# Optimization experiments

Hardware: AMD Instinct MI355X
Metric: run time of the kernel (lower is better)

## Reference

```python
import jax, jax.numpy as jnp
import numpy as np

NUM_HEADS = 32
NUM_KV_HEADS = 8
HEAD_DIM = 128
ROPE_BASE = 10000.0


def _rope_tables(seq_len, head_dim, dtype):
    inv_freq = 1.0 / (ROPE_BASE ** (jnp.arange(0, head_dim, 2, dtype=jnp.float32) / head_dim))
    t = jnp.arange(seq_len, dtype=jnp.float32)
    freqs = jnp.einsum('i,j->ij', t, inv_freq)          # [S, D/2]
    emb = jnp.concatenate([freqs, freqs], axis=-1)      # [S, D]
    return jnp.cos(emb).astype(dtype), jnp.sin(emb).astype(dtype)


def _rotate_half(x):
    x1, x2 = jnp.split(x, 2, axis=-1)
    return jnp.concatenate([-x2, x1], axis=-1)


def _apply_rope(x, cos, sin):
    # x: [B, H, S, D]; cos/sin: [S, D] broadcast over batch and heads
    return x * cos[None, None, :, :] + _rotate_half(x) * sin[None, None, :, :]


def setup_inputs() -> dict:
    key = jax.random.key(0)
    k1, k2, k3, k4, k5 = jax.random.split(key, 5)
    B, S, H = 1, 2048, 4096
    scale = 0.02
    return {
        'hidden_states': jax.random.normal(k1, (B, S, H), dtype=jnp.float32),
        'Wq': jax.random.normal(k2, (4096, 4096), dtype=jnp.float32) * scale,
        'Wk': jax.random.normal(k3, (1024, 4096), dtype=jnp.float32) * scale,
        'Wv': jax.random.normal(k4, (1024, 4096), dtype=jnp.float32) * scale,
        'Wo': jax.random.normal(k5, (4096, 4096), dtype=jnp.float32) * scale,
    }


def reference(hidden_states, Wq, Wk, Wv, Wo):
    B, S, hidden = hidden_states.shape
    n_rep = NUM_HEADS // NUM_KV_HEADS

    # projections (torch Linear: y = x @ W.T)
    q = (hidden_states @ Wq.T).reshape(B, S, NUM_HEADS, HEAD_DIM).transpose(0, 2, 1, 3)
    k = (hidden_states @ Wk.T).reshape(B, S, NUM_KV_HEADS, HEAD_DIM).transpose(0, 2, 1, 3)
    v = (hidden_states @ Wv.T).reshape(B, S, NUM_KV_HEADS, HEAD_DIM).transpose(0, 2, 1, 3)

    # RoPE: init path with no past -> query/key position ids both arange(S)
    cos, sin = _rope_tables(S, HEAD_DIM, hidden_states.dtype)
    q = _apply_rope(q, cos, sin)
    k = _apply_rope(k, cos, sin)

    # repeat_kv: [B, Hkv, S, D] -> [B, H, S, D]
    k = jnp.repeat(k, n_rep, axis=1)
    v = jnp.repeat(v, n_rep, axis=1)

    # manual attention with causal mask
    scores = jnp.einsum('bhqd,bhkd->bhqk', q, k) / jnp.sqrt(jnp.float32(HEAD_DIM)).astype(q.dtype)
    causal = jnp.tril(jnp.ones((S, S), dtype=bool))
    scores = jnp.where(causal[None, None, :, :], scores, jnp.finfo(scores.dtype).min)
    probs = jax.nn.softmax(scores, axis=-1)

    out = jnp.einsum('bhqk,bhkd->bhqd', probs, v)        # [B, H, S, D]
    out = out.transpose(0, 2, 1, 3).reshape(B, S, hidden)
    return out @ Wo.T
```

## Files before the change

### kernel.cpp

```cpp
#include <hip/hip_runtime.h>
#include <hip/hip_bf16.h>

typedef __attribute__((ext_vector_type(4))) float f32x4;
typedef __attribute__((ext_vector_type(8))) short short8;
typedef __attribute__((ext_vector_type(4))) unsigned int u32x4;

__device__ __forceinline__ unsigned short f2bf(float f) {
  union { float f; unsigned int u; } v; v.f = f;
  unsigned int r = (v.u + 0x7fffu + ((v.u >> 16) & 1u)) >> 16;
  return (unsigned short)r;
}
__device__ __forceinline__ unsigned short f2bf_fast(float f) {
  __hip_bfloat16 h = __float2bfloat16(f);
  return __builtin_bit_cast(unsigned short, h);
}
__device__ __forceinline__ float bf2f(unsigned short h) {
  union { unsigned int u; float f; } v; v.u = ((unsigned int)h) << 16;
  return v.f;
}
__device__ __forceinline__ unsigned int cvt_pk_bf16(float lo, float hi) {
  unsigned int r;
  asm("v_cvt_pk_bf16_f32 %0, %1, %2" : "=v"(r) : "v"(lo), "v"(hi));
  return r;
}

__device__ __forceinline__ void gload_lds16(const void* g, void* l) {
  __builtin_amdgcn_global_load_lds((const __attribute__((address_space(1))) void*)g,
                                   (__attribute__((address_space(3))) void*)l,
                                   16, 0, 0);
}

template <int N>
__device__ __forceinline__ void vmwait() {
  asm volatile("s_waitcnt vmcnt(%0)" :: "n"(N) : "memory");
}

__global__ __launch_bounds__(256) void cvt_all(
    const float* __restrict__ hid, const float* __restrict__ wq,
    const float* __restrict__ wk, const float* __restrict__ wv,
    const float* __restrict__ wo, unsigned short* __restrict__ out) {
  const size_t E0 = 8388608, E1 = 25165824, E2 = 29360128, E3 = 33554432, E4 = 50331648;
  size_t stride = (size_t)gridDim.x * blockDim.x;
  for (size_t i = (size_t)blockIdx.x * blockDim.x + threadIdx.x; i * 4 < E4; i += stride) {
    size_t i4 = i * 4;
    const float* src; size_t rel;
    if (i4 < E0)      { src = hid; rel = i4; }
    else if (i4 < E1) { src = wq;  rel = i4 - E0; }
    else if (i4 < E2) { src = wk;  rel = i4 - E1; }
    else if (i4 < E3) { src = wv;  rel = i4 - E2; }
    else              { src = wo;  rel = i4 - E3; }
    float4 v = *(const float4*)(src + rel);
    ushort4 o;
    o.x = f2bf(v.x); o.y = f2bf(v.y); o.z = f2bf(v.z); o.w = f2bf(v.w);
    *(ushort4*)(out + i4) = o;
  }
}

template <int BM, int BN, bool BF16_OUT>
__global__ __launch_bounds__(256, 2) void gemm_p2(
    const unsigned short* __restrict__ A,
    const unsigned short* __restrict__ B,
    void* __restrict__ Cout, int M, int N, int K) {
  constexpr int BK = 64;
  constexpr int MFRAG = BM / 32;
  constexpr int NFRAG = BN / 32;
  constexpr int ASH = BM * BK;
  constexpr int BSH = BN * BK;
  constexpr int BUF = ASH + BSH;
  constexpr int ALOADS = BM / 32;
  constexpr int BLOADS = BN / 32;
  __shared__ unsigned short lds[2 * BUF];

  const int tid = threadIdx.x;
  const int wave = tid >> 6, lane = tid & 63;
  const int l15 = lane & 15, l4 = lane >> 4;
  const int row0 = blockIdx.y * BM, col0 = blockIdx.x * BN;
  const int mrow0 = (wave >> 1) * (BM / 2);
  const int ncol0 = (wave & 1) * (BN / 2);
  const int NT = K >> 6;
  const int srow = tid >> 3;
  const int scol = ((tid & 7) ^ (srow & 7)) * 8;

  f32x4 zv = {0.f, 0.f, 0.f, 0.f};
  f32x4 acc[MFRAG][NFRAG];
#pragma unroll
  for (int m = 0; m < MFRAG; ++m)
#pragma unroll
    for (int n = 0; n < NFRAG; ++n) acc[m][n] = zv;

  auto stage = [&](int t) {
    unsigned short* buf = &lds[(t & 1) * BUF];
    const int k0 = t * BK;
#pragma unroll
    for (int i = 0; i < ALOADS; ++i)
      gload_lds16(A + (size_t)(row0 + i * 32 + srow) * K + k0 + scol,
                  buf + i * 2048 + tid * 8);
#pragma unroll
    for (int i = 0; i < BLOADS; ++i)
      gload_lds16(B + (size_t)(col0 + i * 32 + srow) * K + k0 + scol,
                  buf + ASH + i * 2048 + tid * 8);
  };

  stage(0);

  for (int t = 0; t < NT; ++t) {
    vmwait<0>();
    __builtin_amdgcn_sched_barrier(0);
    __builtin_amdgcn_s_barrier();
    __builtin_amdgcn_sched_barrier(0);
    if (t + 1 < NT) stage(t + 1);

    const unsigned short* Ab = &lds[(t & 1) * BUF];
    const unsigned short* Bb = Ab + ASH;
#pragma unroll
    for (int h = 0; h < 2; ++h) {
      short8 afr[MFRAG], bfr[NFRAG];
#pragma unroll
      for (int m = 0; m < MFRAG; ++m) {
        int row = mrow0 + m * 16 + l15;
        afr[m] = *(const short8*)&Ab[row * 64 + (((h * 4 + l4) ^ (l15 & 7)) * 8)];
      }
#pragma unroll
      for (int n = 0; n < NFRAG; ++n) {
        int row = ncol0 + n * 16 + l15;
        bfr[n] = *(const short8*)&Bb[row * 64 + (((h * 4 + l4) ^ (l15 & 7)) * 8)];
      }
      __builtin_amdgcn_s_setprio(1);
#pragma unroll
      for (int m = 0; m < MFRAG; ++m)
#pragma unroll
        for (int n = 0; n < NFRAG; ++n)
          acc[m][n] = __builtin_amdgcn_mfma_f32_16x16x32_bf16(afr[m], bfr[n], acc[m][n], 0, 0, 0);
      __builtin_amdgcn_s_setprio(0);
    }
    __builtin_amdgcn_sched_barrier(0);
  }

#pragma unroll
  for (int m = 0; m < MFRAG; ++m)
#pragma unroll
    for (int n = 0; n < NFRAG; ++n)
#pragma unroll
      for (int j = 0; j < 4; ++j) {
        int r = row0 + mrow0 + m * 16 + l4 * 4 + j;
        int cc = col0 + ncol0 + n * 16 + l15;
        if constexpr (BF16_OUT)
          ((unsigned short*)Cout)[(size_t)r * N + cc] = f2bf(acc[m][n][j]);
        else
          ((float*)Cout)[(size_t)r * N + cc] = acc[m][n][j];
      }
}

__global__ __launch_bounds__(256) void rope_k(unsigned short* __restrict__ QKV) {
  int idx = blockIdx.x * blockDim.x + threadIdx.x;
  if (idx >= 2048 * 40 * 64) return;
  int j = idx & 63;
  int rest = idx >> 6;
  int slot = rest % 40;
  int s = rest / 40;
  int doff = (slot < 32) ? slot * 128 : 4096 + (slot - 32) * 128;
  unsigned short* p = QKV + (size_t)s * 6144 + doff;
  float inv = exp2f((float)j * -0.20762050593046015f);
  float ang = (float)s * inv;
  float sn, cs;
  sincosf(ang, &sn, &cs);
  float x1 = bf2f(p[j]), x2 = bf2f(p[j + 64]);
  p[j]      = f2bf(x1 * cs - x2 * sn);
  p[j + 64] = f2bf(x2 * cs + x1 * sn);
}

__global__ __launch_bounds__(512, 4) void attn_k(
    const unsigned short* __restrict__ QKV,
    unsigned short* __restrict__ O) {
  __shared__ unsigned short Ks[2][64 * 128];
  __shared__ unsigned short Vs[2][64 * 128];

  const int tid = threadIdx.x;
  const int wave = tid >> 6, lane = tid & 63;
  const int l15 = lane & 15, l4 = lane >> 4;

  const int bid = blockIdx.x;
  const int qt16 = bid & 15;
  const int h = (bid >> 4) & 31;
  const int qt = (h < 16) ? (15 - qt16) : qt16;
  const int hkv = h >> 2;
  const int q0 = qt * 128;
  const int qrow = q0 + wave * 16 + l15;
  const float C2 = 0.12751744219938793f;

  const unsigned short* Qp = QKV + h * 128;
  const unsigned short* Kp = QKV + 4096 + hkv * 128;
  const unsigned short* Vp = QKV + 5120 + hkv * 128;

  const int vpr = tid >> 4;
  const int vd8 = tid & 15;
  const int vg8 = vpr >> 2, vjj = 2 * (vpr & 3);
  const int vn = vd8 >> 1, vch = (vd8 & 1) * 8;

  short8 qf[4];
#pragma unroll
  for (int kc = 0; kc < 4; ++kc)
    qf[kc] = *(const short8*)(Qp + (size_t)qrow * 6144 + kc * 32 + l4 * 8);

  f32x4 zv = {0.f, 0.f, 0.f, 0.f};
  f32x4 oacc[8];
#pragma unroll
  for (int n = 0; n < 8; ++n) oacc[n] = zv;
  float mrow = -3.0e38f, lrow = 0.f;

  auto stageK = [&](int kvn, int b) {
#pragma unroll
    for (int i = 0; i < 2; ++i) {
      int c = wave * 2 + i;
      int row = c * 4 + l4;
      int colel = (l15 * 8) ^ ((row & 7) << 3);
      gload_lds16(Kp + (size_t)(kvn + row) * 6144 + colel, &Ks[b][c * 512]);
    }
  };
  auto loadV = [&](int kvn, short8& va, short8& vb) {
    va = *(const short8*)(Vp + (size_t)(kvn + 2 * vpr) * 6144 + vd8 * 8);
    vb = *(const short8*)(Vp + (size_t)(kvn + 2 * vpr + 1) * 6144 + vd8 * 8);
  };
  auto writeV = [&](int b, const short8& va, const short8& vb) {
#pragma unroll
    for (int i = 0; i < 8; ++i) {
      int c = vch + i;
      unsigned int pack = (unsigned int)(unsigned short)va[i] |
                          ((unsigned int)(unsigned short)vb[i] << 16);
      *(unsigned int*)&Vs[b][vg8 * 1024 + vn * 128 + ((c ^ vn) & 15) * 8 + vjj] = pack;
    }
  };

  {
    short8 va, vb;
    stageK(0, 0);
    loadV(0, va, vb);
    writeV(0, va, vb);
  }
  __syncthreads();

  const int nt = 2 * qt + 2;
  for (int t = 0; t < nt; ++t) {
    const int cur = t & 1, nxt = cur ^ 1;
    const int kv0 = t * 64;
    const bool has_next = (t + 1 < nt);
    short8 va, vb;
    if (has_next) {
      stageK(kv0 + 64, nxt);
      loadV(kv0 + 64, va, vb);
    }

    f32x4 sacc[4];
#pragma unroll
    for (int cb = 0; cb < 4; ++cb) sacc[cb] = zv;
    __builtin_amdgcn_s_setprio(1);
#pragma unroll
    for (int cb = 0; cb < 4; ++cb) {
      int row = cb * 16 + l15;
      int sw = (row & 7) << 3;
#pragma unroll
      for (int kc = 0; kc < 4; ++kc) {
        short8 kf = *(const short8*)&Ks[cur][row * 128 + ((kc * 32 + l4 * 8) ^ sw)];
        sacc[cb] = __builtin_amdgcn_mfma_f32_16x16x32_bf16(kf, qf[kc], sacc[cb], 0, 0, 0);
      }
    }
    __builtin_amdgcn_s_setprio(0);

    if (kv0 + 63 > q0 + wave * 16) {
#pragma unroll
      for (int cb = 0; cb < 4; ++cb)
#pragma unroll
        for (int j = 0; j < 4; ++j) {
          int kvpos = kv0 + cb * 16 + l4 * 4 + j;
          if (kvpos > qrow) sacc[cb][j] = -3.0e38f;
        }
    }

    float pm = sacc[0][0];
#pragma unroll
    for (int cb = 0; cb < 4; ++cb)
#pragma unroll
      for (int j = 0; j < 4; ++j) pm = fmaxf(pm, sacc[cb][j]);
    pm = fmaxf(pm, __shfl_xor(pm, 16, 64));
    pm = fmaxf(pm, __shfl_xor(pm, 32, 64));

    if (__any(pm > mrow + 64.0f)) {
      float mn = fmaxf(mrow, pm);
      float rs = exp2f((mrow - mn) * C2);
      mrow = mn;
      lrow *= rs;
      float rs0 = __shfl(rs, 4 * l4 + 0, 64);
      float rs1 = __shfl(rs, 4 * l4 + 1, 64);
      float rs2 = __shfl(rs, 4 * l4 + 2, 64);
      float rs3 = __shfl(rs, 4 * l4 + 3, 64);
#pragma unroll
      for (int n = 0; n < 8; ++n) {
        oacc[n][0] *= rs0; oacc[n][1] *= rs1;
        oacc[n][2] *= rs2; oacc[n][3] *= rs3;
      }
    }

    unsigned int pack[8];
    float psum = 0.f;
#pragma unroll
    for (int cb = 0; cb < 4; ++cb) {
      float p0 = exp2f((sacc[cb][0] - mrow) * C2);
      float p1 = exp2f((sacc[cb][1] - mrow) * C2);
      float p2 = exp2f((sacc[cb][2] - mrow) * C2);
      float p3 = exp2f((sacc[cb][3] - mrow) * C2);
      psum += (p0 + p1) + (p2 + p3);
      pack[cb * 2 + 0] = cvt_pk_bf16(p0, p1);
      pack[cb * 2 + 1] = cvt_pk_bf16(p2, p3);
    }
    lrow += psum;

#pragma unroll
    for (int ks = 0; ks < 2; ++ks) {
      u32x4 pw;
#pragma unroll
      for (int w = 0; w < 4; ++w) {
        int sl = l15 + 16 * ((2 * l4 + (w >> 1)) & 3);
        int v0 = __shfl((int)pack[4 * ks + (w & 1)], sl, 64);
        int v1 = __shfl((int)pack[4 * ks + 2 + (w & 1)], sl, 64);
        pw[w] = (lane < 32) ? (unsigned int)v0 : (unsigned int)v1;
      }
      short8 pf = __builtin_bit_cast(short8, pw);
      __builtin_amdgcn_s_setprio(1);
#pragma unroll
      for (int n = 0; n < 8; ++n) {
        short8 vf = *(const short8*)&Vs[cur][(ks * 4 + l4) * 1024 + n * 128 + ((l15 ^ n) & 15) * 8];
        oacc[n] = __builtin_amdgcn_mfma_f32_16x16x32_bf16(pf, vf, oacc[n], 0, 0, 0);
      }
      __builtin_amdgcn_s_setprio(0);
    }

    if (has_next) writeV(nxt, va, vb);
    __syncthreads();
  }

  lrow += __shfl_xor(lrow, 16, 64);
  lrow += __shfl_xor(lrow, 32, 64);
  float linv = 1.0f / lrow;
  float li0 = __shfl(linv, 4 * l4 + 0, 64);
  float li1 = __shfl(linv, 4 * l4 + 1, 64);
  float li2 = __shfl(linv, 4 * l4 + 2, 64);
  float li3 = __shfl(linv, 4 * l4 + 3, 64);
#pragma unroll
  for (int n = 0; n < 8; ++n) {
    int r = q0 + wave * 16 + l4 * 4;
    size_t base = (size_t)r * 4096 + h * 128 + n * 16 + l15;
    O[base]          = f2bf_fast(oacc[n][0] * li0);
    O[base + 4096]   = f2bf_fast(oacc[n][1] * li1);
    O[base + 8192]   = f2bf_fast(oacc[n][2] * li2);
    O[base + 12288]  = f2bf_fast(oacc[n][3] * li3);
  }
}

extern "C" void kernel_launch(void* const* d_in, const int* in_sizes, int n_in,
                              void* d_out, int out_size, void* d_ws, size_t ws_size,
                              hipStream_t stream) {
  const float* hid = (const float*)d_in[0];
  const float* Wq  = (const float*)d_in[1];
  const float* Wk  = (const float*)d_in[2];
  const float* Wv  = (const float*)d_in[3];
  const float* Wo  = (const float*)d_in[4];

  char* ws = (char*)d_ws;
  size_t off = 0;
  unsigned short* hid_b = (unsigned short*)(ws + off); off += (size_t)2048 * 4096 * 2;
  unsigned short* Wq_b  = (unsigned short*)(ws + off); off += (size_t)4096 * 4096 * 2;
  unsigned short* Wk_b  = (unsigned short*)(ws + off); off += (size_t)1024 * 4096 * 2;
  unsigned short* Wv_b  = (unsigned short*)(ws + off); off += (size_t)1024 * 4096 * 2;
  unsigned short* Wo_b  = (unsigned short*)(ws + off); off += (size_t)4096 * 4096 * 2;
  unsigned short* QKV   = (unsigned short*)(ws + off); off += (size_t)2048 * 6144 * 2;
  unsigned short* Ob    = (unsigned short*)(ws + off); off += (size_t)2048 * 4096 * 2;
  (void)Wk_b; (void)Wv_b;

  cvt_all<<<4096, 256, 0, stream>>>(hid, Wq, Wk, Wv, Wo, hid_b);

  gemm_p2<128, 192, true><<<dim3(32, 16), 256, 0, stream>>>(hid_b, Wq_b, (void*)QKV, 2048, 6144, 4096);

  rope_k<<<20480, 256, 0, stream>>>(QKV);

  attn_k<<<512, 512, 0, stream>>>(QKV, Ob);

  gemm_p2<128, 128, false><<<dim3(32, 16), 256, 0, stream>>>(Ob, Wo_b, d_out, 2048, 4096, 4096);
}
```

Before: 317.2 us.

## Single-buffer K/V LDS tiles with register prefetch to raise attention occupancy

The attention kernel drops double-buffered LDS for K and V, halving shared memory per block, and raises the launch-bounds occupancy hint from 4 to 6 blocks. K is now prefetched into registers with ordinary global loads and written to LDS after the compute, replacing the direct global-to-LDS loads. A second barrier per iteration protects the single buffer. The block-to-(head, q-tile) mapping is also changed so the heaviest causal tiles across all heads are scheduled first. The trade-off is more registers per thread, an extra sync per KV tile, and tighter register limits from the higher occupancy target.

```diff
diff --git a/kernel.cpp b/kernel.cpp
--- a/kernel.cpp
+++ b/kernel.cpp
@@ -169,20 +169,19 @@
   p[j + 64] = f2bf(x2 * cs + x1 * sn);
 }
 
-__global__ __launch_bounds__(512, 4) void attn_k(
+__global__ __launch_bounds__(512, 6) void attn_k(
     const unsigned short* __restrict__ QKV,
     unsigned short* __restrict__ O) {
-  __shared__ unsigned short Ks[2][64 * 128];
-  __shared__ unsigned short Vs[2][64 * 128];
+  __shared__ unsigned short Ks[64 * 128];
+  __shared__ unsigned short Vs[64 * 128];
 
   const int tid = threadIdx.x;
   const int wave = tid >> 6, lane = tid & 63;
   const int l15 = lane & 15, l4 = lane >> 4;
 
   const int bid = blockIdx.x;
-  const int qt16 = bid & 15;
-  const int h = (bid >> 4) & 31;
-  const int qt = (h < 16) ? (15 - qt16) : qt16;
+  const int qt = 15 - (bid >> 5);
+  const int h = bid & 31;
   const int hkv = h >> 2;
   const int q0 = qt * 128;
   const int qrow = q0 + wave * 16 + l15;
@@ -192,6 +191,8 @@
   const unsigned short* Kp = QKV + 4096 + hkv * 128;
   const unsigned short* Vp = QKV + 5120 + hkv * 128;
 
+  const int krow = tid >> 3, ks8 = tid & 7;
+  const int ksw = (ks8 ^ (krow & 7)) * 8;
   const int vpr = tid >> 4;
   const int vd8 = tid & 15;
   const int vg8 = vpr >> 2, vjj = 2 * (vpr & 3);
@@ -208,45 +209,45 @@
   for (int n = 0; n < 8; ++n) oacc[n] = zv;
   float mrow = -3.0e38f, lrow = 0.f;
 
-  auto stageK = [&](int kvn, int b) {
-#pragma unroll
-    for (int i = 0; i < 2; ++i) {
-      int c = wave * 2 + i;
-      int row = c * 4 + l4;
-      int colel = (l15 * 8) ^ ((row & 7) << 3);
-      gload_lds16(Kp + (size_t)(kvn + row) * 6144 + colel, &Ks[b][c * 512]);
-    }
+  auto loadK = [&](int kvn, short8& k0, short8& k1) {
+    const unsigned short* p = Kp + (size_t)(kvn + krow) * 6144 + ks8 * 8;
+    k0 = *(const short8*)p;
+    k1 = *(const short8*)(p + 64);
+  };
+  auto writeK = [&](const short8& k0, const short8& k1) {
+    *(short8*)&Ks[krow * 128 + ksw] = k0;
+    *(short8*)&Ks[krow * 128 + 64 + ksw] = k1;
   };
   auto loadV = [&](int kvn, short8& va, short8& vb) {
     va = *(const short8*)(Vp + (size_t)(kvn + 2 * vpr) * 6144 + vd8 * 8);
     vb = *(const short8*)(Vp + (size_t)(kvn + 2 * vpr + 1) * 6144 + vd8 * 8);
   };
-  auto writeV = [&](int b, const short8& va, const short8& vb) {
+  auto writeV = [&](const short8& va, const short8& vb) {
 #pragma unroll
     for (int i = 0; i < 8; ++i) {
       int c = vch + i;
       unsigned int pack = (unsigned int)(unsigned short)va[i] |
                           ((unsigned int)(unsigned short)vb[i] << 16);
-      *(unsigned int*)&Vs[b][vg8 * 1024 + vn * 128 + ((c ^ vn) & 15) * 8 + vjj] = pack;
+      *(unsigned int*)&Vs[vg8 * 1024 + vn * 128 + ((c ^ vn) & 15) * 8 + vjj] = pack;
     }
   };
 
   {
-    short8 va, vb;
-    stageK(0, 0);
+    short8 k0, k1, va, vb;
+    loadK(0, k0, k1);
     loadV(0, va, vb);
-    writeV(0, va, vb);
+    writeK(k0, k1);
+    writeV(va, vb);
   }
   __syncthreads();
 
   const int nt = 2 * qt + 2;
   for (int t = 0; t < nt; ++t) {
-    const int cur = t & 1, nxt = cur ^ 1;
     const int kv0 = t * 64;
     const bool has_next = (t + 1 < nt);
-    short8 va, vb;
+    short8 k0, k1, va, vb;
     if (has_next) {
-      stageK(kv0 + 64, nxt);
+      loadK(kv0 + 64, k0, k1);
       loadV(kv0 + 64, va, vb);
     }
 
@@ -260,7 +261,7 @@
       int sw = (row & 7) << 3;
 #pragma unroll
       for (int kc = 0; kc < 4; ++kc) {
-        short8 kf = *(const short8*)&Ks[cur][row * 128 + ((kc * 32 + l4 * 8) ^ sw)];
+        short8 kf = *(const short8*)&Ks[row * 128 + ((kc * 32 + l4 * 8) ^ sw)];
         sacc[cb] = __builtin_amdgcn_mfma_f32_16x16x32_bf16(kf, qf[kc], sacc[cb], 0, 0, 0);
       }
     }
@@ -328,14 +329,18 @@
       __builtin_amdgcn_s_setprio(1);
 #pragma unroll
       for (int n = 0; n < 8; ++n) {
-        short8 vf = *(const short8*)&Vs[cur][(ks * 4 + l4) * 1024 + n * 128 + ((l15 ^ n) & 15) * 8];
+        short8 vf = *(const short8*)&Vs[(ks * 4 + l4) * 1024 + n * 128 + ((l15 ^ n) & 15) * 8];
         oacc[n] = __builtin_amdgcn_mfma_f32_16x16x32_bf16(pf, vf, oacc[n], 0, 0, 0);
       }
       __builtin_amdgcn_s_setprio(0);
     }
 
-    if (has_next) writeV(nxt, va, vb);
     __syncthreads();
+    if (has_next) {
+      writeK(k0, k1);
+      writeV(va, vb);
+      __syncthreads();
+    }
   }
 
   lrow += __shfl_xor(lrow, 16, 64);
```

New measurement: 541.9 us. 70.8% more time.

## Fuse fp32-to-bf16 weight conversion into GEMM B-tile loads

Applied to the files above, without the earlier changes.

Drops the separate weight conversion pass and has the GEMMs load fp32 weights directly, converting them to bf16 in registers before writing to LDS. Wq/Wk/Wv are selected by row range so the QKV GEMM reads the three weight tensors without concatenation. This removes the full write and re-read of bf16 weight copies, at the cost of doubling B-tile global traffic per GEMM and replacing async global-to-LDS loads with register-staged loads.

```diff
diff --git a/kernel.cpp b/kernel.cpp
--- a/kernel.cpp
+++ b/kernel.cpp
@@ -35,31 +35,23 @@
   asm volatile("s_waitcnt vmcnt(%0)" :: "n"(N) : "memory");
 }
 
-__global__ __launch_bounds__(256) void cvt_all(
-    const float* __restrict__ hid, const float* __restrict__ wq,
-    const float* __restrict__ wk, const float* __restrict__ wv,
-    const float* __restrict__ wo, unsigned short* __restrict__ out) {
-  const size_t E0 = 8388608, E1 = 25165824, E2 = 29360128, E3 = 33554432, E4 = 50331648;
+__global__ __launch_bounds__(256) void cvt_hid(const float* __restrict__ in,
+                                               unsigned short* __restrict__ out,
+                                               int n) {
   size_t stride = (size_t)gridDim.x * blockDim.x;
-  for (size_t i = (size_t)blockIdx.x * blockDim.x + threadIdx.x; i * 4 < E4; i += stride) {
-    size_t i4 = i * 4;
-    const float* src; size_t rel;
-    if (i4 < E0)      { src = hid; rel = i4; }
-    else if (i4 < E1) { src = wq;  rel = i4 - E0; }
-    else if (i4 < E2) { src = wk;  rel = i4 - E1; }
-    else if (i4 < E3) { src = wv;  rel = i4 - E2; }
-    else              { src = wo;  rel = i4 - E3; }
-    float4 v = *(const float4*)(src + rel);
+  for (size_t i = (size_t)blockIdx.x * blockDim.x + threadIdx.x; i * 4 < (size_t)n; i += stride) {
+    float4 v = *(const float4*)(in + i * 4);
     ushort4 o;
     o.x = f2bf(v.x); o.y = f2bf(v.y); o.z = f2bf(v.z); o.w = f2bf(v.w);
-    *(ushort4*)(out + i4) = o;
+    *(ushort4*)(out + i * 4) = o;
   }
 }
 
 template <int BM, int BN, bool BF16_OUT>
-__global__ __launch_bounds__(256, 2) void gemm_p2(
+__global__ __launch_bounds__(256, 2) void gemm_f32b(
     const unsigned short* __restrict__ A,
-    const unsigned short* __restrict__ B,
+    const float* __restrict__ B0, const float* __restrict__ B1,
+    const float* __restrict__ B2, int b1, int b2,
     void* __restrict__ Cout, int M, int N, int K) {
   constexpr int BK = 64;
   constexpr int MFRAG = BM / 32;
@@ -79,7 +71,7 @@
   const int ncol0 = (wave & 1) * (BN / 2);
   const int NT = K >> 6;
   const int srow = tid >> 3;
-  const int scol = ((tid & 7) ^ (srow & 7)) * 8;
+  const int spsw = (tid & 7) ^ (srow & 7);
 
   f32x4 zv = {0.f, 0.f, 0.f, 0.f};
   f32x4 acc[MFRAG][NFRAG];
@@ -88,27 +80,55 @@
 #pragma unroll
     for (int n = 0; n < NFRAG; ++n) acc[m][n] = zv;
 
-  auto stage = [&](int t) {
+  float4 br[2 * BLOADS];
+
+  auto stageA = [&](int t) {
     unsigned short* buf = &lds[(t & 1) * BUF];
     const int k0 = t * BK;
 #pragma unroll
     for (int i = 0; i < ALOADS; ++i)
-      gload_lds16(A + (size_t)(row0 + i * 32 + srow) * K + k0 + scol,
+      gload_lds16(A + (size_t)(row0 + i * 32 + srow) * K + k0 + spsw * 8,
                   buf + i * 2048 + tid * 8);
-#pragma unroll
-    for (int i = 0; i < BLOADS; ++i)
-      gload_lds16(B + (size_t)(col0 + i * 32 + srow) * K + k0 + scol,
-                  buf + ASH + i * 2048 + tid * 8);
-  };
-
-  stage(0);
+  };
+  auto loadB = [&](int t) {
+    const int k0 = t * BK;
+#pragma unroll
+    for (int i = 0; i < BLOADS; ++i) {
+      int grow = col0 + i * 32;
+      const float* src; int rrow;
+      if (grow < b1)      { src = B0; rrow = grow; }
+      else if (grow < b2) { src = B1; rrow = grow - b1; }
+      else                { src = B2; rrow = grow - b2; }
+      const float* p = src + (size_t)(rrow + srow) * K + k0 + spsw * 8;
+      br[2 * i]     = *(const float4*)p;
+      br[2 * i + 1] = *(const float4*)(p + 4);
+    }
+  };
+  auto writeB = [&](int t) {
+    unsigned short* buf = &lds[(t & 1) * BUF];
+#pragma unroll
+    for (int i = 0; i < BLOADS; ++i) {
+      u32x4 w;
+      w[0] = cvt_pk_bf16(br[2 * i].x, br[2 * i].y);
+      w[1] = cvt_pk_bf16(br[2 * i].z, br[2 * i].w);
+      w[2] = cvt_pk_bf16(br[2 * i + 1].x, br[2 * i + 1].y);
+      w[3] = cvt_pk_bf16(br[2 * i + 1].z, br[2 * i + 1].w);
+      *(u32x4*)&buf[ASH + i * 2048 + tid * 8] = w;
+    }
+  };
+
+  stageA(0);
+  loadB(0);
+  vmwait<0>();
+  writeB(0);
 
   for (int t = 0; t < NT; ++t) {
-    vmwait<0>();
+    asm volatile("s_waitcnt lgkmcnt(0)" ::: "memory");
     __builtin_amdgcn_sched_barrier(0);
     __builtin_amdgcn_s_barrier();
     __builtin_amdgcn_sched_barrier(0);
-    if (t + 1 < NT) stage(t + 1);
+    const bool hn = (t + 1 < NT);
+    if (hn) { stageA(t + 1); loadB(t + 1); }
 
     const unsigned short* Ab = &lds[(t & 1) * BUF];
     const unsigned short* Bb = Ab + ASH;
@@ -133,7 +153,12 @@
           acc[m][n] = __builtin_amdgcn_mfma_f32_16x16x32_bf16(afr[m], bfr[n], acc[m][n], 0, 0, 0);
       __builtin_amdgcn_s_setprio(0);
     }
-    __builtin_amdgcn_sched_barrier(0);
+
+    if (hn) {
+      vmwait<0>();
+      __builtin_amdgcn_sched_barrier(0);
+      writeB(t + 1);
+    }
   }
 
 #pragma unroll
@@ -368,21 +393,18 @@
   char* ws = (char*)d_ws;
   size_t off = 0;
   unsigned short* hid_b = (unsigned short*)(ws + off); off += (size_t)2048 * 4096 * 2;
-  unsigned short* Wq_b  = (unsigned short*)(ws + off); off += (size_t)4096 * 4096 * 2;
-  unsigned short* Wk_b  = (unsigned short*)(ws + off); off += (size_t)1024 * 4096 * 2;
-  unsigned short* Wv_b  = (unsigned short*)(ws + off); off += (size_t)1024 * 4096 * 2;
-  unsigned short* Wo_b  = (unsigned short*)(ws + off); off += (size_t)4096 * 4096 * 2;
   unsigned short* QKV   = (unsigned short*)(ws + off); off += (size_t)2048 * 6144 * 2;
   unsigned short* Ob    = (unsigned short*)(ws + off); off += (size_t)2048 * 4096 * 2;
-  (void)Wk_b; (void)Wv_b;
-
-  cvt_all<<<4096, 256, 0, stream>>>(hid, Wq, Wk, Wv, Wo, hid_b);
-
-  gemm_p2<128, 192, true><<<dim3(32, 16), 256, 0, stream>>>(hid_b, Wq_b, (void*)QKV, 2048, 6144, 4096);
+
+  cvt_hid<<<2048, 256, 0, stream>>>(hid, hid_b, 2048 * 4096);
+
+  gemm_f32b<128, 192, true><<<dim3(32, 16), 256, 0, stream>>>(
+      hid_b, Wq, Wk, Wv, 4096, 5120, (void*)QKV, 2048, 6144, 4096);
 
   rope_k<<<20480, 256, 0, stream>>>(QKV);
 
   attn_k<<<512, 512, 0, stream>>>(QKV, Ob);
 
-  gemm_p2<128, 128, false><<<dim3(32, 16), 256, 0, stream>>>(Ob, Wo_b, d_out, 2048, 4096, 4096);
-}
+  gemm_f32b<128, 128, false><<<dim3(32, 16), 256, 0, stream>>>(
+      Ob, Wo, Wo, Wo, 4096, 4096, d_out, 2048, 4096, 4096);
+}
```

Result: no change. 318.8 us (+0.5%).

## Split attention KV range into two halves and merge partial outputs

Applied to the files above, without the earlier changes.

Each (head, query tile) block now splits its causal KV range into two equal halves handled by separate blocks. Each block writes a normalized partial output plus its row max and sum, and a new merge kernel combines them with softmax rescaling. This doubles the grid to 1024 blocks, in heaviest-first order, to improve load balance and occupancy. The cost is an extra kernel launch, extra global traffic for the partial outputs, and an extra bf16 rounding step. Partial buffers reuse the Wq/Wk bf16 workspace regions, which are no longer needed after the QKV GEMM.

```diff
diff --git a/kernel.cpp b/kernel.cpp
--- a/kernel.cpp
+++ b/kernel.cpp
@@ -169,9 +169,10 @@
   p[j + 64] = f2bf(x2 * cs + x1 * sn);
 }
 
-__global__ __launch_bounds__(512, 4) void attn_k(
+__global__ __launch_bounds__(512, 4) void attn_part(
     const unsigned short* __restrict__ QKV,
-    unsigned short* __restrict__ O) {
+    unsigned short* __restrict__ Opart,
+    float* __restrict__ ML) {
   __shared__ unsigned short Ks[2][64 * 128];
   __shared__ unsigned short Vs[2][64 * 128];
 
@@ -180,9 +181,10 @@
   const int l15 = lane & 15, l4 = lane >> 4;
 
   const int bid = blockIdx.x;
-  const int qt16 = bid & 15;
-  const int h = (bid >> 4) & 31;
-  const int qt = (h < 16) ? (15 - qt16) : qt16;
+  const int qt = 15 - (bid >> 6);
+  const int rest = bid & 63;
+  const int h = rest >> 1;
+  const int half = rest & 1;
   const int hkv = h >> 2;
   const int q0 = qt * 128;
   const int qrow = q0 + wave * 16 + l15;
@@ -231,19 +233,21 @@
     }
   };
 
+  const int t0 = half * (qt + 1);
+  const int t1 = t0 + (qt + 1);
+
   {
     short8 va, vb;
-    stageK(0, 0);
-    loadV(0, va, vb);
-    writeV(0, va, vb);
+    stageK(t0 * 64, t0 & 1);
+    loadV(t0 * 64, va, vb);
+    writeV(t0 & 1, va, vb);
   }
   __syncthreads();
 
-  const int nt = 2 * qt + 2;
-  for (int t = 0; t < nt; ++t) {
+  for (int t = t0; t < t1; ++t) {
     const int cur = t & 1, nxt = cur ^ 1;
     const int kv0 = t * 64;
-    const bool has_next = (t + 1 < nt);
+    const bool has_next = (t + 1 < t1);
     short8 va, vb;
     if (has_next) {
       stageK(kv0 + 64, nxt);
@@ -340,20 +344,51 @@
 
   lrow += __shfl_xor(lrow, 16, 64);
   lrow += __shfl_xor(lrow, 32, 64);
+  if (l4 == 0) {
+    int r = q0 + wave * 16 + l15;
+    *(float2*)&ML[((size_t)half * 2048 + r) * 64 + h * 2] = make_float2(mrow, lrow);
+  }
   float linv = 1.0f / lrow;
   float li0 = __shfl(linv, 4 * l4 + 0, 64);
   float li1 = __shfl(linv, 4 * l4 + 1, 64);
   float li2 = __shfl(linv, 4 * l4 + 2, 64);
   float li3 = __shfl(linv, 4 * l4 + 3, 64);
+  unsigned short* Oh = Opart + (size_t)half * 2048 * 4096;
 #pragma unroll
   for (int n = 0; n < 8; ++n) {
     int r = q0 + wave * 16 + l4 * 4;
     size_t base = (size_t)r * 4096 + h * 128 + n * 16 + l15;
-    O[base]          = f2bf_fast(oacc[n][0] * li0);
-    O[base + 4096]   = f2bf_fast(oacc[n][1] * li1);
-    O[base + 8192]   = f2bf_fast(oacc[n][2] * li2);
-    O[base + 12288]  = f2bf_fast(oacc[n][3] * li3);
-  }
+    Oh[base]          = f2bf_fast(oacc[n][0] * li0);
+    Oh[base + 4096]   = f2bf_fast(oacc[n][1] * li1);
+    Oh[base + 8192]   = f2bf_fast(oacc[n][2] * li2);
+    Oh[base + 12288]  = f2bf_fast(oacc[n][3] * li3);
+  }
+}
+
+__global__ __launch_bounds__(256) void merge_k(
+    const unsigned short* __restrict__ Opart, const float* __restrict__ ML,
+    unsigned short* __restrict__ Ob) {
+  int idx = blockIdx.x * 256 + threadIdx.x;
+  int d8 = idx & 15;
+  int rest = idx >> 4;
+  int h = rest & 31;
+  int r = rest >> 5;
+  const float C2 = 0.12751744219938793f;
+  float2 ml0 = *(const float2*)&ML[(size_t)r * 64 + h * 2];
+  float2 ml1 = *(const float2*)&ML[((size_t)2048 + r) * 64 + h * 2];
+  float m = fmaxf(ml0.x, ml1.x);
+  float w0 = ml0.y * exp2f((ml0.x - m) * C2);
+  float w1 = ml1.y * exp2f((ml1.x - m) * C2);
+  float inv = 1.0f / (w0 + w1);
+  w0 *= inv; w1 *= inv;
+  size_t off = (size_t)r * 4096 + h * 128 + d8 * 8;
+  short8 a = *(const short8*)(Opart + off);
+  short8 b = *(const short8*)(Opart + (size_t)2048 * 4096 + off);
+  short8 o;
+#pragma unroll
+  for (int i = 0; i < 8; ++i)
+    o[i] = (short)f2bf_fast(w0 * bf2f((unsigned short)a[i]) + w1 * bf2f((unsigned short)b[i]));
+  *(short8*)(Ob + off) = o;
 }
 
 extern "C" void kernel_launch(void* const* d_in, const int* in_sizes, int n_in,
@@ -374,7 +409,10 @@
   unsigned short* Wo_b  = (unsigned short*)(ws + off); off += (size_t)4096 * 4096 * 2;
   unsigned short* QKV   = (unsigned short*)(ws + off); off += (size_t)2048 * 6144 * 2;
   unsigned short* Ob    = (unsigned short*)(ws + off); off += (size_t)2048 * 4096 * 2;
-  (void)Wk_b; (void)Wv_b;
+  (void)Wv_b;
+
+  unsigned short* Opart = Wq_b;
+  float*          MLb   = (float*)Wk_b;
 
   cvt_all<<<4096, 256, 0, stream>>>(hid, Wq, Wk, Wv, Wo, hid_b);
 
@@ -382,7 +420,8 @@
 
   rope_k<<<20480, 256, 0, stream>>>(QKV);
 
-  attn_k<<<512, 512, 0, stream>>>(QKV, Ob);
+  attn_part<<<1024, 512, 0, stream>>>(QKV, Opart, MLb);
+  merge_k<<<4096, 256, 0, stream>>>(Opart, MLb, Ob);
 
   gemm_p2<128, 128, false><<<dim3(32, 16), 256, 0, stream>>>(Ob, Wo_b, d_out, 2048, 4096, 4096);
 }
```

Result: faster. 306.7 us (-3.3%).
